# Performance work log

Hardware: AMD Instinct MI355X
Metric: run time of the kernel (lower is better)

Reference implementation:

```python
import jax, jax.numpy as jnp
import numpy as np

N = 50000      # nodes
E = 400000     # edges per relation
R = 3          # edge types
D = 128        # input_dim == hidden_dim
H = 8          # attention heads
Dh = D // H    # per-head dim (16)
OUT = 1        # output logits
NEG_SLOPE = 0.2
LN_EPS = 1e-5


def setup_inputs() -> dict:
    key = jax.random.key(0)
    ks = jax.random.split(key, 20)
    s = 0.05
    f32 = jnp.float32
    return {
        "feat": jax.random.normal(ks[0], (N, D), f32),
        "edge_src": jax.random.randint(ks[1], (R, E), 0, N, dtype=jnp.int32),
        "edge_dst": jax.random.randint(ks[2], (R, E), 0, N, dtype=jnp.int32),
        # conv1: per-relation GATConv params (W, attn_l, attn_r, bias)
        "W1": jax.random.normal(ks[3], (R, D, H * Dh), f32) * s,
        "al1": jax.random.normal(ks[4], (R, H, Dh), f32) * s,
        "ar1": jax.random.normal(ks[5], (R, H, Dh), f32) * s,
        "b1": jnp.zeros((R, H * Dh), f32),
        # conv2
        "W2": jax.random.normal(ks[6], (R, D, H * Dh), f32) * s,
        "al2": jax.random.normal(ks[7], (R, H, Dh), f32) * s,
        "ar2": jax.random.normal(ks[8], (R, H, Dh), f32) * s,
        "b2": jnp.zeros((R, H * Dh), f32),
        # LayerNorm
        "ln_g": jnp.ones((D,), f32),
        "ln_b": jnp.zeros((D,), f32),
        # classifier MLP (dropout inactive at eval)
        "Wc1": jax.random.normal(ks[9], (D, D), f32) * s,
        "bc1": jnp.zeros((D,), f32),
        "Wc2": jax.random.normal(ks[10], (D, OUT), f32) * s,
        "bc2": jnp.zeros((OUT,), f32),
    }


def _gat(x, src, dst, W, al, ar, b):
    """DGL GATConv on one relation: x [N,Din] -> [N, H*Dh]."""
    h = (x @ W).reshape(N, H, Dh)                       # projected feats
    el = (h * al).sum(-1)                               # [N,H] src attn term
    er = (h * ar).sum(-1)                               # [N,H] dst attn term
    e = jax.nn.leaky_relu(el[src] + er[dst], NEG_SLOPE)  # [E,H]
    # edge-softmax over incoming edges per dst node, per head
    m = jax.ops.segment_max(e, dst, num_segments=N)     # [N,H]
    ex = jnp.exp(e - m[dst])
    denom = jax.ops.segment_sum(ex, dst, num_segments=N)
    alpha = ex / denom[dst]                             # [E,H]
    msg = alpha[:, :, None] * h[src]                    # [E,H,Dh]
    out = jax.ops.segment_sum(msg, dst, num_segments=N)  # [N,H,Dh]
    return out.reshape(N, H * Dh) + b


def _hetero(x, edge_src, edge_dst, W, al, ar, b):
    out = jnp.zeros((N, H * Dh), x.dtype)
    for r in range(R):  # small fixed relation count
        out = out + _gat(x, edge_src[r], edge_dst[r], W[r], al[r], ar[r], b[r])
    return out


def reference(feat, edge_src, edge_dst, W1, al1, ar1, b1, W2, al2, ar2, b2,
              ln_g, ln_b, Wc1, bc1, Wc2, bc2):
    h1 = jax.nn.relu(_hetero(feat, edge_src, edge_dst, W1, al1, ar1, b1))
    h2 = _hetero(h1, edge_src, edge_dst, W2, al2, ar2, b2)
    h = h2 + h1
    mu = h.mean(-1, keepdims=True)
    var = ((h - mu) ** 2).mean(-1, keepdims=True)
    h = (h - mu) * jax.lax.rsqrt(var + LN_EPS) * ln_g + ln_b
    h = jax.nn.relu(h @ Wc1 + bc1)
    return h @ Wc2 + bc2
```

## Files before the change

### kernel.cpp

```cpp
#include <hip/hip_runtime.h>
#include <math.h>

#define NN 50000
#define NE 400000
#define NREL 3
#define CAP 32
#define EQ 300000

typedef __bf16 bf16x8 __attribute__((ext_vector_type(8)));
typedef float floatx4 __attribute__((ext_vector_type(4)));

__device__ __forceinline__ unsigned short f2bf(float f) {
  unsigned int u = __float_as_uint(f);
  return (unsigned short)((u + 0x7fffu + ((u >> 16) & 1u)) >> 16);
}
__device__ __forceinline__ float bflo(unsigned int u) {
  return __uint_as_float(u << 16);
}
__device__ __forceinline__ float bfhi(unsigned int u) {
  return __uint_as_float(u & 0xffff0000u);
}

__global__ __launch_bounds__(256) void prep_wt(
    const float* __restrict__ W1, const float* __restrict__ W2,
    const float* __restrict__ Wc1, unsigned short* __restrict__ Wt) {
  int mat = blockIdx.x >> 3, slab = blockIdx.x & 7;
  const float* Wsrc = mat < 3 ? W1 + mat * 16384
                    : (mat < 6 ? W2 + (mat - 3) * 16384 : Wc1);
  unsigned short* dst = Wt + (size_t)mat * 144 * 128;
  int k0 = slab * 16;
#pragma unroll
  for (int i = 0; i < 8; ++i) {
    int idx = i * 256 + threadIdx.x;
    int k = k0 + (idx >> 7), nn = idx & 127;
    dst[nn * 128 + k] = f2bf(Wsrc[k * 128 + nn]);
  }
}

__global__ __launch_bounds__(256) void prep_attn(
    const float* __restrict__ W1, const float* __restrict__ W2,
    const float* __restrict__ al1, const float* __restrict__ ar1,
    const float* __restrict__ al2, const float* __restrict__ ar2,
    unsigned short* __restrict__ Wt) {
  int mat = blockIdx.x;
  const float* Wsrc = mat < 3 ? W1 + mat * 16384 : W2 + (mat - 3) * 16384;
  const float* alp = mat < 3 ? al1 + mat * 128 : al2 + (mat - 3) * 128;
  const float* arp = mat < 3 ? ar1 + mat * 128 : ar2 + (mat - 3) * 128;
  unsigned short* dst = Wt + (size_t)mat * 144 * 128;
#pragma unroll
  for (int i = 0; i < 8; ++i) {
    int j = i * 256 + threadIdx.x;
    int half = j >> 10, jj = j & 1023;
    int k = jj >> 3, h = jj & 7;
    const float* av = half ? arp : alp;
    float s = 0.f;
#pragma unroll
    for (int d = 0; d < 16; ++d) s += Wsrc[k * 128 + h * 16 + d] * av[h * 16 + d];
    dst[(128 + half * 8 + h) * 128 + k] = f2bf(s);
  }
}

__global__ __launch_bounds__(256) void gemm3_attn_mfma(
    const float* __restrict__ X, const unsigned short* __restrict__ Wt,
    unsigned short* __restrict__ hp, float* __restrict__ el,
    float* __restrict__ er, int n) {
  __shared__ unsigned short Xs[64 * 136];
  __shared__ unsigned short Ws[144 * 136];
  int t = threadIdx.x;
  int rowbase = blockIdx.x * 64;

  const float4* X4 = (const float4*)X;
#pragma unroll
  for (int i = 0; i < 8; ++i) {
    int v = t + i * 256;
    int row = v >> 5, k4 = (v & 31) * 4;
    float4 x = make_float4(0.f, 0.f, 0.f, 0.f);
    if (rowbase + row < n) x = X4[(size_t)(rowbase + row) * 32 + (v & 31)];
    ushort4 p;
    p.x = f2bf(x.x); p.y = f2bf(x.y); p.z = f2bf(x.z); p.w = f2bf(x.w);
    *(ushort4*)&Xs[row * 136 + k4] = p;
  }

  int lane = t & 63, wave = t >> 6;
  int quad = lane >> 4, l = lane & 15;

  for (int r = 0; r < NREL; ++r) {
    __syncthreads();
    const uint4* WtR = (const uint4*)(Wt + (size_t)r * 144 * 128);
#pragma unroll
    for (int i = 0; i < 9; ++i) {
      int v = t + i * 256;
      ((uint4*)Ws)[(v >> 4) * 17 + (v & 15)] = WtR[v];
    }
    __syncthreads();

    floatx4 acc[9];
#pragma unroll
    for (int i = 0; i < 9; ++i) acc[i] = floatx4{0.f, 0.f, 0.f, 0.f};
#pragma unroll
    for (int ks = 0; ks < 4; ++ks) {
      bf16x8 a = *(const bf16x8*)&Xs[(wave * 16 + l) * 136 + ks * 32 + quad * 8];
#pragma unroll
      for (int nt = 0; nt < 9; ++nt) {
        bf16x8 b = *(const bf16x8*)&Ws[(nt * 16 + l) * 136 + ks * 32 + quad * 8];
        acc[nt] = __builtin_amdgcn_mfma_f32_16x16x32_bf16(a, b, acc[nt], 0, 0, 0);
      }
    }

    unsigned short* hpR = hp + (size_t)r * NN * 128;
    float* elR = el + (size_t)r * NN * 8;
    float* erR = er + (size_t)r * NN * 8;
    int r0 = rowbase + wave * 16 + quad * 4;
#pragma unroll
    for (int reg = 0; reg < 4; ++reg) {
      int row = r0 + reg;
      if (row < n) {
#pragma unroll
        for (int nt = 0; nt < 8; ++nt)
          hpR[(size_t)row * 128 + nt * 16 + l] = f2bf(acc[nt][reg]);
        if (l < 8) elR[row * 8 + l] = acc[8][reg];
        else       erR[row * 8 + (l - 8)] = acc[8][reg];
      }
    }
  }
}

__global__ __launch_bounds__(256) void gemm_head_mfma(
    const float* __restrict__ X, const unsigned short* __restrict__ Wt,
    const float* __restrict__ bc1, const float* __restrict__ wc2,
    const float* __restrict__ bc2, float* __restrict__ out, int n) {
  __shared__ unsigned short Xs[64 * 136];
  __shared__ unsigned short Ws[128 * 136];
  int t = threadIdx.x;
  int rowbase = blockIdx.x * 64;

  const float4* X4 = (const float4*)X;
#pragma unroll
  for (int i = 0; i < 8; ++i) {
    int v = t + i * 256;
    int row = v >> 5, k4 = (v & 31) * 4;
    float4 x = make_float4(0.f, 0.f, 0.f, 0.f);
    if (rowbase + row < n) x = X4[(size_t)(rowbase + row) * 32 + (v & 31)];
    ushort4 p;
    p.x = f2bf(x.x); p.y = f2bf(x.y); p.z = f2bf(x.z); p.w = f2bf(x.w);
    *(ushort4*)&Xs[row * 136 + k4] = p;
  }
  const uint4* WtR = (const uint4*)Wt;
#pragma unroll
  for (int i = 0; i < 8; ++i) {
    int v = t + i * 256;
    ((uint4*)Ws)[(v >> 4) * 17 + (v & 15)] = WtR[v];
  }
  __syncthreads();

  int lane = t & 63, wave = t >> 6;
  int quad = lane >> 4, l = lane & 15;

  floatx4 acc[8];
#pragma unroll
  for (int i = 0; i < 8; ++i) acc[i] = floatx4{0.f, 0.f, 0.f, 0.f};
#pragma unroll
  for (int ks = 0; ks < 4; ++ks) {
    bf16x8 a = *(const bf16x8*)&Xs[(wave * 16 + l) * 136 + ks * 32 + quad * 8];
#pragma unroll
    for (int nt = 0; nt < 8; ++nt) {
      bf16x8 b = *(const bf16x8*)&Ws[(nt * 16 + l) * 136 + ks * 32 + quad * 8];
      acc[nt] = __builtin_amdgcn_mfma_f32_16x16x32_bf16(a, b, acc[nt], 0, 0, 0);
    }
  }

  float bv[8], wv[8];
#pragma unroll
  for (int nt = 0; nt < 8; ++nt) {
    bv[nt] = bc1[nt * 16 + l];
    wv[nt] = wc2[nt * 16 + l];
  }
  int r0 = rowbase + wave * 16 + quad * 4;
#pragma unroll
  for (int reg = 0; reg < 4; ++reg) {
    float s = 0.f;
#pragma unroll
    for (int nt = 0; nt < 8; ++nt)
      s += fmaxf(acc[nt][reg] + bv[nt], 0.f) * wv[nt];
    s += __shfl_xor(s, 1); s += __shfl_xor(s, 2);
    s += __shfl_xor(s, 4); s += __shfl_xor(s, 8);
    int row = r0 + reg;
    if (l == 0 && row < n) out[row] = s + bc2[0];
  }
}

__global__ __launch_bounds__(256) void build_ell(
    const int* __restrict__ esrc, const int* __restrict__ edst,
    int* __restrict__ cnt, int* __restrict__ colE) {
  int t = blockIdx.x * 256 + threadIdx.x;
  if (t >= EQ) return;
  int d[4], s[4], r[4];
#pragma unroll
  for (int k = 0; k < 4; ++k) {
    int tt = t + k * EQ;
    r[k] = tt / NE;
    d[k] = edst[tt];
    s[k] = esrc[tt];
  }
#pragma unroll
  for (int k = 0; k < 4; ++k) {
    int pos = atomicAdd(&cnt[r[k] * NN + d[k]], 1);
    colE[((size_t)r[k] * NN + d[k]) * CAP + pos] = s[k];
  }
}

__global__ __launch_bounds__(256) void gather_all(
    const int* __restrict__ cnt, const int* __restrict__ colE,
    const float* __restrict__ el, const float* __restrict__ er,
    const unsigned short* __restrict__ hp, const float* __restrict__ b,
    float* __restrict__ h1, const float* __restrict__ g,
    const float* __restrict__ beta, int mode) {
  int wid = (blockIdx.x * 256 + threadIdx.x) >> 6;
  int lane = threadIdx.x & 63;
  if (wid >= NN) return;
  int p = lane >> 5;
  int q = lane & 31;
  int head = q >> 2;
  float ax = 0.f, ay = 0.f, az = 0.f, aw = 0.f;
#pragma unroll
  for (int r = 0; r < NREL; ++r) {
    int deg = cnt[r * NN + wid];
    if (deg <= 0) continue;
    const int* cl = colE + ((size_t)r * NN + wid) * CAP;
    const float* elr = el + (size_t)r * NN * 8;
    const unsigned short* hpr = hp + (size_t)r * NN * 128;
    float er_d = er[(size_t)r * NN * 8 + wid * 8 + head];
    int last = deg - 1;
    float den = 0.f, f0 = 0.f, f1 = 0.f, f2 = 0.f, f3 = 0.f;
    for (int i = 0; i < deg; i += 4) {
      int i0 = i + p, i1 = i + 2 + p;
      int s0 = cl[min(i0, last)];
      int s1 = cl[min(i1, last)];
      float e0 = elr[s0 * 8 + head] + er_d;
      float e1 = elr[s1 * 8 + head] + er_d;
      uint2 u0 = *(const uint2*)&hpr[(size_t)s0 * 128 + q * 4];
      uint2 u1 = *(const uint2*)&hpr[(size_t)s1 * 128 + q * 4];
      e0 = (e0 > 0.f) ? e0 : 0.2f * e0;
      e1 = (e1 > 0.f) ? e1 : 0.2f * e1;
      float x0 = (i0 < deg) ? __expf(e0) : 0.f;
      float x1 = (i1 < deg) ? __expf(e1) : 0.f;
      den += x0 + x1;
      f0 += x0 * bflo(u0.x) + x1 * bflo(u1.x);
      f1 += x0 * bfhi(u0.x) + x1 * bfhi(u1.x);
      f2 += x0 * bflo(u0.y) + x1 * bflo(u1.y);
      f3 += x0 * bfhi(u0.y) + x1 * bfhi(u1.y);
    }
    den += __shfl_xor(den, 32);
    float inv = 1.f / den;
    ax += f0 * inv; ay += f1 * inv; az += f2 * inv; aw += f3 * inv;
  }
  ax += __shfl_xor(ax, 32); ay += __shfl_xor(ay, 32);
  az += __shfl_xor(az, 32); aw += __shfl_xor(aw, 32);

  int c = q * 4;
  float4 b0 = *(const float4*)&b[c];
  float4 bb1 = *(const float4*)&b[128 + c];
  float4 bb2 = *(const float4*)&b[256 + c];
  float vx = ax + b0.x + bb1.x + bb2.x;
  float vy = ay + b0.y + bb1.y + bb2.y;
  float vz = az + b0.z + bb1.z + bb2.z;
  float vw = aw + b0.w + bb1.w + bb2.w;
  float4* hptr = (float4*)&h1[(size_t)wid * 128 + c];
  if (mode == 0) {
    if (p == 0)
      *hptr = make_float4(fmaxf(vx, 0.f), fmaxf(vy, 0.f),
                          fmaxf(vz, 0.f), fmaxf(vw, 0.f));
  } else {
    float4 r1 = *hptr;
    vx += r1.x; vy += r1.y; vz += r1.z; vw += r1.w;
    float s = vx + vy + vz + vw;
    s += __shfl_xor(s, 1); s += __shfl_xor(s, 2);
    s += __shfl_xor(s, 4); s += __shfl_xor(s, 8); s += __shfl_xor(s, 16);
    float mu = s * (1.f / 128.f);
    float dx = vx - mu, dy = vy - mu, dz = vz - mu, dw = vw - mu;
    float sq = dx * dx + dy * dy + dz * dz + dw * dw;
    sq += __shfl_xor(sq, 1); sq += __shfl_xor(sq, 2);
    sq += __shfl_xor(sq, 4); sq += __shfl_xor(sq, 8); sq += __shfl_xor(sq, 16);
    float rstd = rsqrtf(sq * (1.f / 128.f) + 1e-5f);
    float4 gv = *(const float4*)&g[c];
    float4 bv = *(const float4*)&beta[c];
    if (p == 0)
      *hptr = make_float4(dx * rstd * gv.x + bv.x, dy * rstd * gv.y + bv.y,
                          dz * rstd * gv.z + bv.z, dw * rstd * gv.w + bv.w);
  }
}

extern "C" void kernel_launch(void* const* d_in, const int* in_sizes, int n_in,
                              void* d_out, int out_size, void* d_ws, size_t ws_size,
                              hipStream_t stream) {
  const float* feat = (const float*)d_in[0];
  const int* esrc = (const int*)d_in[1];
  const int* edst = (const int*)d_in[2];
  const float* W1 = (const float*)d_in[3];
  const float* al1 = (const float*)d_in[4];
  const float* ar1 = (const float*)d_in[5];
  const float* b1 = (const float*)d_in[6];
  const float* W2 = (const float*)d_in[7];
  const float* al2 = (const float*)d_in[8];
  const float* ar2 = (const float*)d_in[9];
  const float* b2 = (const float*)d_in[10];
  const float* lng = (const float*)d_in[11];
  const float* lnb = (const float*)d_in[12];
  const float* Wc1 = (const float*)d_in[13];
  const float* bc1 = (const float*)d_in[14];
  const float* Wc2 = (const float*)d_in[15];
  const float* bc2 = (const float*)d_in[16];
  float* out = (float*)d_out;

  unsigned short* hp = (unsigned short*)d_ws;
  float* el = (float*)(hp + (size_t)3 * NN * 128);
  float* er = el + (size_t)3 * NN * 8;
  float* h1 = er + (size_t)3 * NN * 8;
  int* cnt = (int*)(h1 + (size_t)NN * 128);
  int* colE = cnt + NREL * NN;
  unsigned short* Wt = (unsigned short*)(colE + (size_t)NREL * NN * CAP);

  const int gemm_grid = (NN + 63) / 64;
  const int edge_grid = (EQ + 255) / 256;
  const int gg_grid = (NN * 64) / 256;

  prep_wt<<<56, 256, 0, stream>>>(W1, W2, Wc1, Wt);
  prep_attn<<<6, 256, 0, stream>>>(W1, W2, al1, ar1, al2, ar2, Wt);

  hipMemsetAsync(cnt, 0, (size_t)NREL * NN * sizeof(int), stream);
  build_ell<<<edge_grid, 256, 0, stream>>>(esrc, edst, cnt, colE);

  gemm3_attn_mfma<<<gemm_grid, 256, 0, stream>>>(feat, Wt, hp, el, er, NN);
  gather_all<<<gg_grid, 256, 0, stream>>>(cnt, colE, el, er, hp, b1,
                                          h1, nullptr, nullptr, 0);
  gemm3_attn_mfma<<<gemm_grid, 256, 0, stream>>>(
      h1, Wt + (size_t)3 * 144 * 128, hp, el, er, NN);
  gather_all<<<gg_grid, 256, 0, stream>>>(cnt, colE, el, er, hp, b2,
                                          h1, lng, lnb, 1);
  gemm_head_mfma<<<gemm_grid, 256, 0, stream>>>(
      h1, Wt + (size_t)6 * 144 * 128, bc1, Wc2, bc2, out, NN);
}
```

Before: 399.4 us.

## Store ELL neighbor indices as 16-bit and pad with sentinel node

Neighbor indices in the ELL table are narrowed from int32 to uint16, which is valid because the node count fits in 16 bits. This halves index storage and lets each wave read four indices with one ushort4 load. Unused slots are pre-filled with a sentinel node whose el entry is set to -1e30, so its exp weight is zero and the per-edge clamp and bounds checks in the gather loop can go. The cost is a new fill kernel that writes the whole padded table instead of a small memset, plus a dependence on the sentinel's hp row holding finite values, since that row is never written.

```diff
diff --git a/kernel.cpp b/kernel.cpp
--- a/kernel.cpp
+++ b/kernel.cpp
@@ -2,10 +2,12 @@
 #include <math.h>
 
 #define NN 50000
+#define NNP 50001
 #define NE 400000
 #define NREL 3
 #define CAP 32
 #define EQ 300000
+#define SENT 50000
 
 typedef __bf16 bf16x8 __attribute__((ext_vector_type(8)));
 typedef float floatx4 __attribute__((ext_vector_type(4)));
@@ -41,8 +43,10 @@
     const float* __restrict__ W1, const float* __restrict__ W2,
     const float* __restrict__ al1, const float* __restrict__ ar1,
     const float* __restrict__ al2, const float* __restrict__ ar2,
-    unsigned short* __restrict__ Wt) {
+    unsigned short* __restrict__ Wt, float* __restrict__ el) {
   int mat = blockIdx.x;
+  if (mat < 3 && threadIdx.x < 8)
+    el[(size_t)mat * NNP * 8 + (size_t)NN * 8 + threadIdx.x] = -1e30f;
   const float* Wsrc = mat < 3 ? W1 + mat * 16384 : W2 + (mat - 3) * 16384;
   const float* alp = mat < 3 ? al1 + mat * 128 : al2 + (mat - 3) * 128;
   const float* arp = mat < 3 ? ar1 + mat * 128 : ar2 + (mat - 3) * 128;
@@ -107,8 +111,8 @@
       }
     }
 
-    unsigned short* hpR = hp + (size_t)r * NN * 128;
-    float* elR = el + (size_t)r * NN * 8;
+    unsigned short* hpR = hp + (size_t)r * NNP * 128;
+    float* elR = el + (size_t)r * NNP * 8;
     float* erR = er + (size_t)r * NN * 8;
     int r0 = rowbase + wave * 16 + quad * 4;
 #pragma unroll
@@ -189,9 +193,18 @@
   }
 }
 
+__global__ __launch_bounds__(256) void fill_ell(
+    uint4* __restrict__ colE4, int* __restrict__ cnt) {
+  int t = blockIdx.x * 256 + threadIdx.x;
+  const unsigned int S2 = (unsigned)SENT | ((unsigned)SENT << 16);
+  if (t < NREL * NN * CAP / 8)
+    colE4[t] = make_uint4(S2, S2, S2, S2);
+  if (t < NREL * NN) cnt[t] = 0;
+}
+
 __global__ __launch_bounds__(256) void build_ell(
     const int* __restrict__ esrc, const int* __restrict__ edst,
-    int* __restrict__ cnt, int* __restrict__ colE) {
+    int* __restrict__ cnt, unsigned short* __restrict__ colE) {
   int t = blockIdx.x * 256 + threadIdx.x;
   if (t >= EQ) return;
   int d[4], s[4], r[4];
@@ -205,12 +218,12 @@
 #pragma unroll
   for (int k = 0; k < 4; ++k) {
     int pos = atomicAdd(&cnt[r[k] * NN + d[k]], 1);
-    colE[((size_t)r[k] * NN + d[k]) * CAP + pos] = s[k];
+    colE[(((size_t)r[k] * NN + d[k]) << 5) + pos] = (unsigned short)s[k];
   }
 }
 
 __global__ __launch_bounds__(256) void gather_all(
-    const int* __restrict__ cnt, const int* __restrict__ colE,
+    const int* __restrict__ cnt, const unsigned short* __restrict__ colE,
     const float* __restrict__ el, const float* __restrict__ er,
     const unsigned short* __restrict__ hp, const float* __restrict__ b,
     float* __restrict__ h1, const float* __restrict__ g,
@@ -226,24 +239,24 @@
   for (int r = 0; r < NREL; ++r) {
     int deg = cnt[r * NN + wid];
     if (deg <= 0) continue;
-    const int* cl = colE + ((size_t)r * NN + wid) * CAP;
-    const float* elr = el + (size_t)r * NN * 8;
-    const unsigned short* hpr = hp + (size_t)r * NN * 128;
+    const unsigned short* cl = colE + (((size_t)r * NN + wid) << 5);
+    const float* elr = el + (size_t)r * NNP * 8;
+    const unsigned short* hpr = hp + (size_t)r * NNP * 128;
     float er_d = er[(size_t)r * NN * 8 + wid * 8 + head];
-    int last = deg - 1;
+    int degp = (deg + 3) & ~3;
     float den = 0.f, f0 = 0.f, f1 = 0.f, f2 = 0.f, f3 = 0.f;
-    for (int i = 0; i < deg; i += 4) {
-      int i0 = i + p, i1 = i + 2 + p;
-      int s0 = cl[min(i0, last)];
-      int s1 = cl[min(i1, last)];
+    for (int i = 0; i < degp; i += 4) {
+      ushort4 c4 = *(const ushort4*)&cl[i];
+      int s0 = p ? c4.z : c4.x;
+      int s1 = p ? c4.w : c4.y;
       float e0 = elr[s0 * 8 + head] + er_d;
       float e1 = elr[s1 * 8 + head] + er_d;
       uint2 u0 = *(const uint2*)&hpr[(size_t)s0 * 128 + q * 4];
       uint2 u1 = *(const uint2*)&hpr[(size_t)s1 * 128 + q * 4];
       e0 = (e0 > 0.f) ? e0 : 0.2f * e0;
       e1 = (e1 > 0.f) ? e1 : 0.2f * e1;
-      float x0 = (i0 < deg) ? __expf(e0) : 0.f;
-      float x1 = (i1 < deg) ? __expf(e1) : 0.f;
+      float x0 = __expf(e0);
+      float x1 = __expf(e1);
       den += x0 + x1;
       f0 += x0 * bflo(u0.x) + x1 * bflo(u1.x);
       f1 += x0 * bfhi(u0.x) + x1 * bfhi(u1.x);
@@ -313,21 +326,22 @@
   float* out = (float*)d_out;
 
   unsigned short* hp = (unsigned short*)d_ws;
-  float* el = (float*)(hp + (size_t)3 * NN * 128);
-  float* er = el + (size_t)3 * NN * 8;
+  float* el = (float*)(hp + (size_t)3 * NNP * 128);
+  float* er = el + (size_t)3 * NNP * 8;
   float* h1 = er + (size_t)3 * NN * 8;
   int* cnt = (int*)(h1 + (size_t)NN * 128);
-  int* colE = cnt + NREL * NN;
-  unsigned short* Wt = (unsigned short*)(colE + (size_t)NREL * NN * CAP);
+  unsigned short* colE = (unsigned short*)(cnt + NREL * NN);
+  unsigned short* Wt = colE + (size_t)NREL * NN * CAP;
 
   const int gemm_grid = (NN + 63) / 64;
   const int edge_grid = (EQ + 255) / 256;
+  const int fill_grid = (NREL * NN * CAP / 8 + 255) / 256;
   const int gg_grid = (NN * 64) / 256;
 
   prep_wt<<<56, 256, 0, stream>>>(W1, W2, Wc1, Wt);
-  prep_attn<<<6, 256, 0, stream>>>(W1, W2, al1, ar1, al2, ar2, Wt);
-
-  hipMemsetAsync(cnt, 0, (size_t)NREL * NN * sizeof(int), stream);
+  prep_attn<<<6, 256, 0, stream>>>(W1, W2, al1, ar1, al2, ar2, Wt, el);
+
+  fill_ell<<<fill_grid, 256, 0, stream>>>((uint4*)colE, cnt);
   build_ell<<<edge_grid, 256, 0, stream>>>(esrc, edst, cnt, colE);
 
   gemm3_attn_mfma<<<gemm_grid, 256, 0, stream>>>(feat, Wt, hp, el, er, NN);
```

After: 406.1 us. About the same (+1.7%).
